# Optimization experiments

Measured on AMD Instinct MI355X. Metric: run time of the kernel, lower is better.

Reference implementation:

```python
import jax, jax.numpy as jnp
import numpy as np

DEPTH = 24
DLAT = 80      # latent_dim
H = 8          # latent_heads
DH = 64        # latent_dim_head
INNER = H * DH # 512
FFD = 2 * DLAT # FeedForward mult=2 -> 160
B = 64         # hardcoded in forward reshape
N = 128        # hardcoded max_num_nodes
MHD = 20       # multi_hop_max_dist
EF = 3         # edge feature count (meaned over by edge encoder)
EPS = 1e-5


def _ln(x, g, b):
    m = x.mean(-1, keepdims=True)
    v = ((x - m) ** 2).mean(-1, keepdims=True)
    return (x - m) / jnp.sqrt(v + EPS) * g + b


def setup_inputs() -> dict:
    key = jax.random.key(0)
    ks = jax.random.split(key, 24)
    std = 0.02 / np.sqrt(DEPTH)
    inp = {}
    # integer graph inputs
    inp['spatial_pos'] = jax.random.randint(ks[0], (B, N, N), 0, 40, dtype=jnp.int32)
    inp['edge_input'] = jax.random.randint(ks[1], (B, N, N, MHD, EF), 0, 64, dtype=jnp.int32)
    inp['x_nodes'] = jax.random.randint(ks[2], (B, N), 0, 64, dtype=jnp.int32)
    inp['indeg'] = jax.random.randint(ks[3], (B, N), 0, 64, dtype=jnp.int32)
    inp['outdeg'] = jax.random.randint(ks[4], (B, N), 0, 64, dtype=jnp.int32)
    # embedding tables (init_params: Embedding std=0.02)
    inp['atom_emb'] = 0.02 * jax.random.normal(ks[5], (64, DLAT), dtype=jnp.float32)
    inp['indeg_emb'] = 0.02 * jax.random.normal(ks[6], (64, DLAT), dtype=jnp.float32)
    inp['outdeg_emb'] = 0.02 * jax.random.normal(ks[7], (64, DLAT), dtype=jnp.float32)
    inp['edge_emb'] = 0.02 * jax.random.normal(ks[8], (64, 1), dtype=jnp.float32)
    inp['edge_dis_w'] = 0.02 * jax.random.normal(ks[9], (40,), dtype=jnp.float32)
    inp['spatial_emb'] = 0.02 * jax.random.normal(ks[10], (40, 1), dtype=jnp.float32)
    # per-layer stacked params (init_params: Linear std=0.02/sqrt(depth), bias 0)
    inp['ln1_g'] = jnp.ones((DEPTH, DLAT), jnp.float32)
    inp['ln1_b'] = jnp.zeros((DEPTH, DLAT), jnp.float32)
    inp['Wq'] = std * jax.random.normal(ks[11], (DEPTH, DLAT, INNER), dtype=jnp.float32)
    inp['Wkv'] = std * jax.random.normal(ks[12], (DEPTH, DLAT, 2 * INNER), dtype=jnp.float32)
    inp['Wo'] = std * jax.random.normal(ks[13], (DEPTH, INNER, DLAT), dtype=jnp.float32)
    inp['bo'] = jnp.zeros((DEPTH, DLAT), jnp.float32)
    inp['ln2_g'] = jnp.ones((DEPTH, DLAT), jnp.float32)
    inp['ln2_b'] = jnp.zeros((DEPTH, DLAT), jnp.float32)
    inp['W1'] = std * jax.random.normal(ks[14], (DEPTH, DLAT, FFD), dtype=jnp.float32)
    inp['b1'] = jnp.zeros((DEPTH, FFD), jnp.float32)
    inp['W2'] = std * jax.random.normal(ks[15], (DEPTH, FFD, DLAT), dtype=jnp.float32)
    inp['b2'] = jnp.zeros((DEPTH, DLAT), jnp.float32)
    # final head: LayerNorm + Linear(latent_dim, 1)
    inp['lnf_g'] = jnp.ones((DLAT,), jnp.float32)
    inp['lnf_b'] = jnp.zeros((DLAT,), jnp.float32)
    inp['Wf'] = std * jax.random.normal(ks[16], (DLAT, 1), dtype=jnp.float32)
    inp['bf'] = jnp.zeros((1,), jnp.float32)
    return inp


def reference(spatial_pos, edge_input, x_nodes, indeg, outdeg,
              atom_emb, indeg_emb, outdeg_emb, edge_emb, edge_dis_w, spatial_emb,
              ln1_g, ln1_b, Wq, Wkv, Wo, bo, ln2_g, ln2_b, W1, b1, W2, b2,
              lnf_g, lnf_b, Wf, bf):
    # --- graph structural bias ---
    sp_bias = spatial_emb[spatial_pos, 0]                       # [B,N,N]
    sp = jnp.where(spatial_pos == 0, 1, spatial_pos)
    sp = jnp.where(sp > 1, sp - 1, sp)
    sp = jnp.clip(sp, 0, MHD)
    e = edge_emb[edge_input, 0].mean(axis=-1)                   # [B,N,N,MHD] (mean over edge feats)
    e = (e * edge_dis_w[:MHD]).sum(-1) / sp.astype(jnp.float32) # per-hop scale, sum hops, normalize
    bias = e + sp_bias                                          # [B,N,N]
    # --- node embeddings ---
    x = atom_emb[x_nodes] + indeg_emb[indeg] + outdeg_emb[outdeg]  # [B,N,DLAT]
    scale = DH ** -0.5

    def layer(x, p):
        g1, be1, wq, wkv, wo, bo_, g2, be2, w1, bb1, w2, bb2 = p
        h = _ln(x, g1, be1)
        q = (h @ wq).reshape(B, N, H, DH)
        kv = h @ wkv
        k = kv[..., :INNER].reshape(B, N, H, DH)
        v = kv[..., INNER:].reshape(B, N, H, DH)
        sim = jnp.einsum('bihd,bjhd->bhij', q, k) * scale + bias[:, None]
        a = jax.nn.softmax(sim, axis=-1)
        o = jnp.einsum('bhij,bjhd->bihd', a, v).reshape(B, N, INNER)
        x = o @ wo + bo_ + x
        h = _ln(x, g2, be2)
        x = jax.nn.gelu(h @ w1 + bb1, approximate=False) @ w2 + bb2 + x
        return x, None

    x, _ = jax.lax.scan(layer, x, (ln1_g, ln1_b, Wq, Wkv, Wo, bo, ln2_g, ln2_b, W1, b1, W2, b2))
    pooled = x.mean(axis=1)                                     # Reduce 'b n d -> b d'
    return _ln(pooled, lnf_g, lnf_b) @ Wf + bf                  # [B,1]
```

## Files before the change

### kernel.cpp

```cpp
#include <hip/hip_runtime.h>
#include <math.h>

#define BDIM 64
#define NNODE 128
#define DLAT 80
#define NHEAD 8
#define DH 64
#define INNER 512
#define FFD 160
#define DEPTH 24
#define MROWS (BDIM * NNODE)

using bf16x8 = __attribute__((ext_vector_type(8))) short;
using f32x4  = __attribute__((ext_vector_type(4))) float;

#define MFMA(a, b, c) __builtin_amdgcn_mfma_f32_16x16x32_bf16((a), (b), (c), 0, 0, 0)

static __device__ __forceinline__ short f2bf(float f) {
    union { float f; unsigned u; } v; v.f = f;
    unsigned r = v.u + 0x7fffu + ((v.u >> 16) & 1u);
    return (short)(r >> 16);
}

__global__ __launch_bounds__(256) void wconv_kernel(
    const float* __restrict__ in, short* __restrict__ out, int K, int N, int Kp)
{
    __shared__ float t[64][65];
    int L = blockIdx.z;
    const float* src = in + (size_t)L * K * N;
    short* dst = out + (size_t)L * N * Kp;
    int n0 = blockIdx.x * 64, k0 = blockIdx.y * 64;
    int tx = threadIdx.x & 63, ty = threadIdx.x >> 6;
    for (int ki = ty; ki < 64; ki += 4) {
        int k = k0 + ki, n = n0 + tx;
        t[ki][tx] = (k < K && n < N) ? src[(size_t)k * N + n] : 0.f;
    }
    __syncthreads();
    for (int ni = ty; ni < 64; ni += 4) {
        int n = n0 + ni, k = k0 + tx;
        if (n < N && k < Kp) dst[(size_t)n * Kp + k] = f2bf(t[tx][ni]);
    }
}

__global__ __launch_bounds__(256) void bias_kernel(
    const int* __restrict__ spp, const int* __restrict__ ei,
    const float* __restrict__ edge_emb, const float* __restrict__ edw,
    const float* __restrict__ sp_emb, float* __restrict__ biasb)
{
    __shared__ float ee[64], ew[20], se[40];
    int tid = threadIdx.x;
    if (tid < 64) ee[tid] = edge_emb[tid];
    if (tid < 20) ew[tid] = edw[tid];
    if (tid < 40) se[tid] = sp_emb[tid];
    __syncthreads();

    int idx = blockIdx.x * 256 + tid;
    int spv = spp[idx];
    float spb = se[spv];
    int sp = min(20, max(1, spv - 1));

    const int4* p = (const int4*)(ei + (size_t)idx * 60);
    int e[60];
#pragma unroll
    for (int t = 0; t < 15; ++t) {
        int4 v = p[t];
        e[4*t+0] = v.x; e[4*t+1] = v.y; e[4*t+2] = v.z; e[4*t+3] = v.w;
    }
    float acc = 0.f;
#pragma unroll
    for (int m = 0; m < 20; ++m) {
        float s = ee[e[3*m]] + ee[e[3*m+1]] + ee[e[3*m+2]];
        acc += s * ew[m];
    }
    biasb[idx] = acc * (1.0f/3.0f) / (float)sp + spb;
}

__global__ __launch_bounds__(256) void node_emb_kernel(
    const int* __restrict__ xn, const int* __restrict__ ind, const int* __restrict__ outd,
    const float* __restrict__ ae, const float* __restrict__ ie, const float* __restrict__ oe,
    float* __restrict__ x)
{
    int idx = blockIdx.x * 256 + threadIdx.x;
    int e = idx / DLAT, d = idx % DLAT;
    x[idx] = ae[xn[e]*DLAT + d] + ie[ind[e]*DLAT + d] + oe[outd[e]*DLAT + d];
}

__global__ __launch_bounds__(256, 2) void attnfull_kernel(
    const float* __restrict__ xin, const float* __restrict__ biasb,
    const short* __restrict__ Wq_t, const short* __restrict__ Wkv_t,
    const float* __restrict__ g1, const float* __restrict__ be1,
    short* __restrict__ obuf)
{
    extern __shared__ short smem[];
    short* lnx = smem;
    short* qh  = smem + 13312;
    short* kh  = smem + 22528;
    short* vth = smem + 31744;
    short* ph  = smem;

    int tid = threadIdx.x;
    int lane = tid & 63, w = tid >> 6, l15 = lane & 15, lk = lane >> 4;
    int b = blockIdx.x >> 3, h = blockIdx.x & 7;
    const float* xb = xin + (size_t)b * NNODE * DLAT;

    {
        int row = tid >> 1, sub = tid & 1;
        const float* xr = xb + row * DLAT + sub * 40;
        float4 v[10];
#pragma unroll
        for (int i = 0; i < 10; ++i) v[i] = *(const float4*)(xr + i * 4);
        float s = 0.f;
#pragma unroll
        for (int i = 0; i < 10; ++i) s += v[i].x + v[i].y + v[i].z + v[i].w;
        s += __shfl_xor(s, 1);
        float mean = s * 0.0125f;
        float var = 0.f;
#pragma unroll
        for (int i = 0; i < 10; ++i) {
            float d;
            d = v[i].x - mean; var += d * d;
            d = v[i].y - mean; var += d * d;
            d = v[i].z - mean; var += d * d;
            d = v[i].w - mean; var += d * d;
        }
        var += __shfl_xor(var, 1);
        float rstd = 1.0f / sqrtf(var * 0.0125f + 1e-5f);
        short* dst = lnx + row * 104 + sub * 40;
#pragma unroll
        for (int i = 0; i < 10; ++i) {
            int c = sub * 40 + i * 4;
            float4 g4 = *(const float4*)(g1 + c);
            float4 b4 = *(const float4*)(be1 + c);
            short4 o;
            o.x = f2bf((v[i].x - mean) * rstd * g4.x + b4.x);
            o.y = f2bf((v[i].y - mean) * rstd * g4.y + b4.y);
            o.z = f2bf((v[i].z - mean) * rstd * g4.z + b4.z);
            o.w = f2bf((v[i].w - mean) * rstd * g4.w + b4.w);
            *(short4*)(dst + i * 4) = o;
        }
        short4 z4; z4.x = z4.y = z4.z = z4.w = 0;
        *(short4*)(lnx + row * 104 + 80 + sub * 8) = z4;
        *(short4*)(lnx + row * 104 + 84 + sub * 8) = z4;
    }
    __syncthreads();

    {
        bf16x8 a[2][3];
#pragma unroll
        for (int i = 0; i < 2; ++i)
#pragma unroll
            for (int ss = 0; ss < 3; ++ss)
                a[i][ss] = *(const bf16x8*)(lnx + ((w * 2 + i) * 16 + l15) * 104 + lk * 8 + ss * 32);

        {
            f32x4 acc[2][4] = {};
#pragma unroll
            for (int ss = 0; ss < 3; ++ss)
#pragma unroll
                for (int nf = 0; nf < 4; ++nf) {
                    bf16x8 bv = *(const bf16x8*)(Wq_t + (size_t)(h * 64 + nf * 16 + l15) * 96 + lk * 8 + ss * 32);
                    acc[0][nf] = MFMA(a[0][ss], bv, acc[0][nf]);
                    acc[1][nf] = MFMA(a[1][ss], bv, acc[1][nf]);
                }
#pragma unroll
            for (int i = 0; i < 2; ++i)
#pragma unroll
                for (int nf = 0; nf < 4; ++nf)
#pragma unroll
                    for (int r = 0; r < 4; ++r)
                        qh[((w * 2 + i) * 16 + lk * 4 + r) * 72 + nf * 16 + l15] = f2bf(acc[i][nf][r]);
        }
        {
            f32x4 acc[2][4] = {};
#pragma unroll
            for (int ss = 0; ss < 3; ++ss)
#pragma unroll
                for (int nf = 0; nf < 4; ++nf) {
                    bf16x8 bv = *(const bf16x8*)(Wkv_t + (size_t)(h * 64 + nf * 16 + l15) * 96 + lk * 8 + ss * 32);
                    acc[0][nf] = MFMA(a[0][ss], bv, acc[0][nf]);
                    acc[1][nf] = MFMA(a[1][ss], bv, acc[1][nf]);
                }
#pragma unroll
            for (int i = 0; i < 2; ++i)
#pragma unroll
                for (int nf = 0; nf < 4; ++nf)
#pragma unroll
                    for (int r = 0; r < 4; ++r)
                        kh[((w * 2 + i) * 16 + lk * 4 + r) * 72 + nf * 16 + l15] = f2bf(acc[i][nf][r]);
        }
        {
            f32x4 acc[2][4] = {};
#pragma unroll
            for (int ss = 0; ss < 3; ++ss)
#pragma unroll
                for (int nf = 0; nf < 4; ++nf) {
                    bf16x8 bv = *(const bf16x8*)(Wkv_t + (size_t)(INNER + h * 64 + nf * 16 + l15) * 96 + lk * 8 + ss * 32);
                    acc[0][nf] = MFMA(a[0][ss], bv, acc[0][nf]);
                    acc[1][nf] = MFMA(a[1][ss], bv, acc[1][nf]);
                }
#pragma unroll
            for (int i = 0; i < 2; ++i)
#pragma unroll
                for (int nf = 0; nf < 4; ++nf)
#pragma unroll
                    for (int r = 0; r < 4; ++r)
                        vth[(nf * 16 + l15) * 136 + (w * 2 + i) * 16 + lk * 4 + r] = f2bf(acc[i][nf][r]);
        }
    }
    __syncthreads();

    float breg[2][8][4];
    {
        const float* bp = biasb + ((size_t)b * NNODE + w * 32) * NNODE;
#pragma unroll
        for (int i = 0; i < 2; ++i)
#pragma unroll
            for (int jf = 0; jf < 8; ++jf)
#pragma unroll
                for (int r = 0; r < 4; ++r)
                    breg[i][jf][r] = bp[(i * 16 + lk * 4 + r) * NNODE + jf * 16 + l15];
    }

    f32x4 sc[2][8] = {};
#pragma unroll
    for (int ss = 0; ss < 2; ++ss) {
        bf16x8 qa0 = *(const bf16x8*)(qh + ((w * 2) * 16 + l15) * 72 + lk * 8 + ss * 32);
        bf16x8 qa1 = *(const bf16x8*)(qh + ((w * 2 + 1) * 16 + l15) * 72 + lk * 8 + ss * 32);
#pragma unroll
        for (int jf = 0; jf < 8; ++jf) {
            bf16x8 bv = *(const bf16x8*)(kh + (jf * 16 + l15) * 72 + lk * 8 + ss * 32);
            sc[0][jf] = MFMA(qa0, bv, sc[0][jf]);
            sc[1][jf] = MFMA(qa1, bv, sc[1][jf]);
        }
    }
    __syncthreads();

    float rinv[2][4];
#pragma unroll
    for (int i = 0; i < 2; ++i)
#pragma unroll
    for (int r = 0; r < 4; ++r) {
        float sv[8];
#pragma unroll
        for (int jf = 0; jf < 8; ++jf) sv[jf] = sc[i][jf][r] * 0.125f + breg[i][jf][r];
        float mx = sv[0];
#pragma unroll
        for (int jf = 1; jf < 8; ++jf) mx = fmaxf(mx, sv[jf]);
        mx = fmaxf(mx, __shfl_xor(mx, 1));
        mx = fmaxf(mx, __shfl_xor(mx, 2));
        mx = fmaxf(mx, __shfl_xor(mx, 4));
        mx = fmaxf(mx, __shfl_xor(mx, 8));
        float e[8], sum = 0.f;
#pragma unroll
        for (int jf = 0; jf < 8; ++jf) { e[jf] = __expf(sv[jf] - mx); sum += e[jf]; }
        sum += __shfl_xor(sum, 1);
        sum += __shfl_xor(sum, 2);
        sum += __shfl_xor(sum, 4);
        sum += __shfl_xor(sum, 8);
        rinv[i][r] = 1.0f / sum;
        int row = (w * 2 + i) * 16 + lk * 4 + r;
#pragma unroll
        for (int jf = 0; jf < 8; ++jf)
            ph[row * 136 + jf * 16 + l15] = f2bf(e[jf]);
    }
    __syncthreads();

    f32x4 o[2][4] = {};
#pragma unroll
    for (int ks = 0; ks < 4; ++ks) {
        bf16x8 pa0 = *(const bf16x8*)(ph + ((w * 2) * 16 + l15) * 136 + lk * 8 + ks * 32);
        bf16x8 pa1 = *(const bf16x8*)(ph + ((w * 2 + 1) * 16 + l15) * 136 + lk * 8 + ks * 32);
#pragma unroll
        for (int nf = 0; nf < 4; ++nf) {
            bf16x8 bv = *(const bf16x8*)(vth + (nf * 16 + l15) * 136 + lk * 8 + ks * 32);
            o[0][nf] = MFMA(pa0, bv, o[0][nf]);
            o[1][nf] = MFMA(pa1, bv, o[1][nf]);
        }
    }
#pragma unroll
    for (int i = 0; i < 2; ++i)
#pragma unroll
    for (int nf = 0; nf < 4; ++nf)
#pragma unroll
    for (int r = 0; r < 4; ++r) {
        int row = (w * 2 + i) * 16 + lk * 4 + r;
        obuf[((size_t)b * NNODE + row) * INNER + h * 64 + nf * 16 + l15] =
            f2bf(o[i][nf][r] * rinv[i][r]);
    }
}

__global__ __launch_bounds__(512, 2) void tail_kernel(
    const short* __restrict__ obuf, const float* __restrict__ xin,
    const short* __restrict__ Wo_t, const float* __restrict__ boL,
    const float* __restrict__ g2, const float* __restrict__ be2,
    const short* __restrict__ W1_t, const float* __restrict__ b1L,
    const short* __restrict__ W2_t, const float* __restrict__ b2L,
    float* __restrict__ xout)
{
    __shared__ short obs[32 * 520];
    __shared__ float xmid[32 * 84];
    __shared__ short h2s[32 * 104];
    __shared__ short ffhs[32 * 168];

    int tid = threadIdx.x;
    int lane = tid & 63, w = tid >> 6, l15 = lane & 15, lk = lane >> 4;
    int b = blockIdx.x >> 2, qq = blockIdx.x & 3;
    int R0 = qq * 32;
    int wr = w >> 2, wn = w & 3;

    {
        int row = tid >> 4, cs = (tid & 15) * 32;
        const short* src = obuf + ((size_t)b * NNODE + R0 + row) * INNER + cs;
        short* dst = obs + row * 520 + cs;
#pragma unroll
        for (int q = 0; q < 4; ++q)
            *(uint4*)(dst + q * 8) = *(const uint4*)(src + q * 8);
    }
    __syncthreads();

    const int st5[4] = {0, 2, 3, 4}, cn5[4] = {2, 1, 1, 1};
    const int st10[4] = {0, 3, 6, 8}, cn10[4] = {3, 3, 2, 2};

    {
        int n0 = st5[wn], nc = cn5[wn];
        f32x4 acc[2] = {};
#pragma unroll 4
        for (int ks = 0; ks < 16; ++ks) {
            bf16x8 aa = *(const bf16x8*)(obs + (wr * 16 + l15) * 520 + lk * 8 + ks * 32);
#pragma unroll
            for (int j = 0; j < 2; ++j)
                if (j < nc) {
                    bf16x8 bv = *(const bf16x8*)(Wo_t + (size_t)((n0 + j) * 16 + l15) * INNER + lk * 8 + ks * 32);
                    acc[j] = MFMA(aa, bv, acc[j]);
                }
        }
#pragma unroll
        for (int j = 0; j < 2; ++j)
            if (j < nc)
#pragma unroll
                for (int r = 0; r < 4; ++r) {
                    int row = wr * 16 + lk * 4 + r, col = (n0 + j) * 16 + l15;
                    xmid[row * 84 + col] = acc[j][r] + boL[col] +
                        xin[((size_t)b * NNODE + R0 + row) * DLAT + col];
                }
    }
    __syncthreads();

    {
        int row = tid >> 4, sub = tid & 15;
        float v[5];
#pragma unroll
        for (int e = 0; e < 5; ++e) v[e] = xmid[row * 84 + sub * 5 + e];
        float s = v[0] + v[1] + v[2] + v[3] + v[4];
        s += __shfl_xor(s, 1); s += __shfl_xor(s, 2);
        s += __shfl_xor(s, 4); s += __shfl_xor(s, 8);
        float mean = s * 0.0125f;
        float var = 0.f;
#pragma unroll
        for (int e = 0; e < 5; ++e) { float d = v[e] - mean; var += d * d; }
        var += __shfl_xor(var, 1); var += __shfl_xor(var, 2);
        var += __shfl_xor(var, 4); var += __shfl_xor(var, 8);
        float rstd = 1.0f / sqrtf(var * 0.0125f + 1e-5f);
#pragma unroll
        for (int e = 0; e < 5; ++e) {
            int c = sub * 5 + e;
            h2s[row * 104 + c] = f2bf((v[e] - mean) * rstd * g2[c] + be2[c]);
        }
        if (sub < 4) {
            short4 z4; z4.x = z4.y = z4.z = z4.w = 0;
            *(short4*)(h2s + row * 104 + 80 + sub * 4) = z4;
        }
    }
    __syncthreads();

    {
        int n0 = st10[wn], nc = cn10[wn];
        f32x4 acc[3] = {};
#pragma unroll
        for (int ss = 0; ss < 3; ++ss) {
            bf16x8 aa = *(const bf16x8*)(h2s + (wr * 16 + l15) * 104 + lk * 8 + ss * 32);
#pragma unroll
            for (int j = 0; j < 3; ++j)
                if (j < nc) {
                    bf16x8 bv = *(const bf16x8*)(W1_t + (size_t)((n0 + j) * 16 + l15) * 96 + lk * 8 + ss * 32);
                    acc[j] = MFMA(aa, bv, acc[j]);
                }
        }
#pragma unroll
        for (int j = 0; j < 3; ++j)
            if (j < nc)
#pragma unroll
                for (int r = 0; r < 4; ++r) {
                    int row = wr * 16 + lk * 4 + r, c = (n0 + j) * 16 + l15;
                    float vv = acc[j][r] + b1L[c];
                    vv = 0.5f * vv * (1.0f + erff(vv * 0.70710678118654752f));
                    ffhs[row * 168 + c] = f2bf(vv);
                }
    }
    __syncthreads();

    {
        int n0 = st5[wn], nc = cn5[wn];
        f32x4 acc[2] = {};
#pragma unroll
        for (int ks = 0; ks < 5; ++ks) {
            bf16x8 aa = *(const bf16x8*)(ffhs + (wr * 16 + l15) * 168 + lk * 8 + ks * 32);
#pragma unroll
            for (int j = 0; j < 2; ++j)
                if (j < nc) {
                    bf16x8 bv = *(const bf16x8*)(W2_t + (size_t)((n0 + j) * 16 + l15) * FFD + lk * 8 + ks * 32);
                    acc[j] = MFMA(aa, bv, acc[j]);
                }
        }
#pragma unroll
        for (int j = 0; j < 2; ++j)
            if (j < nc)
#pragma unroll
                for (int r = 0; r < 4; ++r) {
                    int row = wr * 16 + lk * 4 + r, col = (n0 + j) * 16 + l15;
                    xout[((size_t)b * NNODE + R0 + row) * DLAT + col] =
                        acc[j][r] + b2L[col] + xmid[row * 84 + col];
                }
    }
}

__global__ __launch_bounds__(128) void final_kernel(
    const float* __restrict__ x, const float* __restrict__ g, const float* __restrict__ bta,
    const float* __restrict__ Wf, const float* __restrict__ bf, float* __restrict__ out)
{
    int bb = blockIdx.x;
    int t = threadIdx.x;
    __shared__ float pd[DLAT];
    __shared__ float red[2];
    __shared__ float rbuf[128];

    if (t < DLAT) {
        float s = 0.f;
        for (int n = 0; n < NNODE; ++n) s += x[((size_t)bb * NNODE + n) * DLAT + t];
        pd[t] = s * (1.0f / NNODE);
    }
    __syncthreads();
    if (t == 0) {
        float m = 0.f;
        for (int k = 0; k < DLAT; ++k) m += pd[k];
        m /= DLAT;
        float v = 0.f;
        for (int k = 0; k < DLAT; ++k) { float d = pd[k] - m; v += d * d; }
        v /= DLAT;
        red[0] = m; red[1] = 1.0f / sqrtf(v + 1e-5f);
    }
    __syncthreads();
    float contrib = 0.f;
    if (t < DLAT)
        contrib = ((pd[t] - red[0]) * red[1] * g[t] + bta[t]) * Wf[t];
    rbuf[t] = contrib;
    __syncthreads();
    if (t == 0) {
        float s = 0.f;
        for (int k = 0; k < DLAT; ++k) s += rbuf[k];
        out[bb] = s + bf[0];
    }
}

extern "C" void kernel_launch(void* const* d_in, const int* in_sizes, int n_in,
                              void* d_out, int out_size, void* d_ws, size_t ws_size,
                              hipStream_t stream)
{
    const int*   spatial_pos = (const int*)  d_in[0];
    const int*   edge_input  = (const int*)  d_in[1];
    const int*   x_nodes     = (const int*)  d_in[2];
    const int*   indeg       = (const int*)  d_in[3];
    const int*   outdeg      = (const int*)  d_in[4];
    const float* atom_emb    = (const float*)d_in[5];
    const float* indeg_emb   = (const float*)d_in[6];
    const float* outdeg_emb  = (const float*)d_in[7];
    const float* edge_emb    = (const float*)d_in[8];
    const float* edge_dis_w  = (const float*)d_in[9];
    const float* spatial_emb = (const float*)d_in[10];
    const float* ln1_g = (const float*)d_in[11];
    const float* ln1_b = (const float*)d_in[12];
    const float* Wq    = (const float*)d_in[13];
    const float* Wkv   = (const float*)d_in[14];
    const float* Wo    = (const float*)d_in[15];
    const float* bo    = (const float*)d_in[16];
    const float* ln2_g = (const float*)d_in[17];
    const float* ln2_b = (const float*)d_in[18];
    const float* W1    = (const float*)d_in[19];
    const float* b1    = (const float*)d_in[20];
    const float* W2    = (const float*)d_in[21];
    const float* b2    = (const float*)d_in[22];
    const float* lnf_g = (const float*)d_in[23];
    const float* lnf_b = (const float*)d_in[24];
    const float* Wf    = (const float*)d_in[25];
    const float* bf    = (const float*)d_in[26];

    char* wsb = (char*)d_ws;
    float* biasb = (float*)(wsb + 0);
    float* x0    = (float*)(wsb + 4194304);
    float* x1    = (float*)(wsb + 6815744);
    short* obuf  = (short*)(wsb + 9437184);
    short* Wq_t  = (short*)(wsb + 17825792);
    short* Wkv_t = (short*)(wsb + 20185088);
    short* Wo_t  = (short*)(wsb + 24903680);
    short* W1_t  = (short*)(wsb + 26869760);
    short* W2_t  = (short*)(wsb + 27607040);

    static const int ATTN_LDS = 80896;
    hipFuncSetAttribute((const void*)attnfull_kernel,
                        hipFuncAttributeMaxDynamicSharedMemorySize, ATTN_LDS);

    wconv_kernel<<<dim3(8, 2, 24), 256, 0, stream>>>(Wq,  Wq_t,  80, 512, 96);
    wconv_kernel<<<dim3(16, 2, 24), 256, 0, stream>>>(Wkv, Wkv_t, 80, 1024, 96);
    wconv_kernel<<<dim3(2, 8, 24), 256, 0, stream>>>(Wo,  Wo_t,  512, 80, 512);
    wconv_kernel<<<dim3(3, 2, 24), 256, 0, stream>>>(W1,  W1_t,  80, 160, 96);
    wconv_kernel<<<dim3(2, 3, 24), 256, 0, stream>>>(W2,  W2_t,  160, 80, 160);

    bias_kernel<<<4096, 256, 0, stream>>>(spatial_pos, edge_input, edge_emb,
                                          edge_dis_w, spatial_emb, biasb);
    node_emb_kernel<<<2560, 256, 0, stream>>>(x_nodes, indeg, outdeg,
                                              atom_emb, indeg_emb, outdeg_emb, x0);

    for (int L = 0; L < DEPTH; ++L) {
        const float* xin  = (L & 1) ? x1 : x0;
        float*       xout = (L & 1) ? x0 : x1;
        attnfull_kernel<<<512, 256, ATTN_LDS, stream>>>(
            xin, biasb,
            Wq_t + (size_t)L * 512 * 96, Wkv_t + (size_t)L * 1024 * 96,
            ln1_g + L * DLAT, ln1_b + L * DLAT, obuf);
        tail_kernel<<<256, 512, 0, stream>>>(
            obuf, xin,
            Wo_t + (size_t)L * 80 * 512, bo + L * DLAT,
            ln2_g + L * DLAT, ln2_b + L * DLAT,
            W1_t + (size_t)L * 160 * 96, b1 + L * FFD,
            W2_t + (size_t)L * 80 * 160, b2 + L * DLAT,
            xout);
    }

    final_kernel<<<BDIM, 128, 0, stream>>>(x0, lnf_g, lnf_b, Wf, bf, (float*)d_out);
}
```

Measured before the change: 1.521 ms.

## Move LN1 into previous layer's tail kernel and widen attention to 512 threads

LayerNorm-1 now runs at the end of the previous layer's tail kernel, or in a new ln1_kernel before the first layer, and writes bf16 normalized activations to a global buffer. The attention kernel no longer normalizes every row once per head and can use less LDS. The attention kernel now runs 8 waves of 16 rows each, with lower per-thread register use and a staged, coalesced output store through LDS. The tail kernel reads obuf directly from global memory instead of staging it in LDS. This trades an extra global lnx buffer and more global A-operand loads in the Wo GEMM for higher occupancy and less redundant LN work.

New measurement: 1.529 ms. Within noise of the previous version (+0.5%).

```diff
diff --git a/kernel.cpp b/kernel.cpp
--- a/kernel.cpp
+++ b/kernel.cpp
@@ -85,164 +85,148 @@
     x[idx] = ae[xn[e]*DLAT + d] + ie[ind[e]*DLAT + d] + oe[outd[e]*DLAT + d];
 }
 
-__global__ __launch_bounds__(256, 2) void attnfull_kernel(
-    const float* __restrict__ xin, const float* __restrict__ biasb,
+__global__ __launch_bounds__(256) void ln1_kernel(
+    const float* __restrict__ x, const float* __restrict__ g,
+    const float* __restrict__ be, short* __restrict__ lnx)
+{
+    int row = blockIdx.x * 128 + (threadIdx.x >> 1), sub = threadIdx.x & 1;
+    const float* xr = x + (size_t)row * DLAT + sub * 40;
+    float4 v[10];
+#pragma unroll
+    for (int i = 0; i < 10; ++i) v[i] = *(const float4*)(xr + i * 4);
+    float s = 0.f;
+#pragma unroll
+    for (int i = 0; i < 10; ++i) s += v[i].x + v[i].y + v[i].z + v[i].w;
+    s += __shfl_xor(s, 1);
+    float mean = s * 0.0125f;
+    float var = 0.f;
+#pragma unroll
+    for (int i = 0; i < 10; ++i) {
+        float d;
+        d = v[i].x - mean; var += d * d;
+        d = v[i].y - mean; var += d * d;
+        d = v[i].z - mean; var += d * d;
+        d = v[i].w - mean; var += d * d;
+    }
+    var += __shfl_xor(var, 1);
+    float rstd = 1.0f / sqrtf(var * 0.0125f + 1e-5f);
+    short* dst = lnx + (size_t)row * 96 + sub * 40;
+#pragma unroll
+    for (int i = 0; i < 10; ++i) {
+        int c = sub * 40 + i * 4;
+        float4 g4 = *(const float4*)(g + c);
+        float4 b4 = *(const float4*)(be + c);
+        short4 o;
+        o.x = f2bf((v[i].x - mean) * rstd * g4.x + b4.x);
+        o.y = f2bf((v[i].y - mean) * rstd * g4.y + b4.y);
+        o.z = f2bf((v[i].z - mean) * rstd * g4.z + b4.z);
+        o.w = f2bf((v[i].w - mean) * rstd * g4.w + b4.w);
+        *(short4*)(dst + i * 4) = o;
+    }
+    short4 z4; z4.x = z4.y = z4.z = z4.w = 0;
+    *(short4*)(lnx + (size_t)row * 96 + 80 + sub * 8) = z4;
+    *(short4*)(lnx + (size_t)row * 96 + 84 + sub * 8) = z4;
+}
+
+__global__ __launch_bounds__(512, 4) void attn2_kernel(
+    const short* __restrict__ lnx, const float* __restrict__ biasb,
     const short* __restrict__ Wq_t, const short* __restrict__ Wkv_t,
-    const float* __restrict__ g1, const float* __restrict__ be1,
     short* __restrict__ obuf)
 {
     extern __shared__ short smem[];
-    short* lnx = smem;
-    short* qh  = smem + 13312;
-    short* kh  = smem + 22528;
-    short* vth = smem + 31744;
+    short* qh  = smem;
+    short* kh  = smem + 9216;
+    short* vth = smem + 18432;
     short* ph  = smem;
+    short* ot  = smem + 18432;
 
     int tid = threadIdx.x;
     int lane = tid & 63, w = tid >> 6, l15 = lane & 15, lk = lane >> 4;
     int b = blockIdx.x >> 3, h = blockIdx.x & 7;
-    const float* xb = xin + (size_t)b * NNODE * DLAT;
-
-    {
-        int row = tid >> 1, sub = tid & 1;
-        const float* xr = xb + row * DLAT + sub * 40;
-        float4 v[10];
-#pragma unroll
-        for (int i = 0; i < 10; ++i) v[i] = *(const float4*)(xr + i * 4);
-        float s = 0.f;
-#pragma unroll
-        for (int i = 0; i < 10; ++i) s += v[i].x + v[i].y + v[i].z + v[i].w;
-        s += __shfl_xor(s, 1);
-        float mean = s * 0.0125f;
-        float var = 0.f;
-#pragma unroll
-        for (int i = 0; i < 10; ++i) {
-            float d;
-            d = v[i].x - mean; var += d * d;
-            d = v[i].y - mean; var += d * d;
-            d = v[i].z - mean; var += d * d;
-            d = v[i].w - mean; var += d * d;
-        }
-        var += __shfl_xor(var, 1);
-        float rstd = 1.0f / sqrtf(var * 0.0125f + 1e-5f);
-        short* dst = lnx + row * 104 + sub * 40;
-#pragma unroll
-        for (int i = 0; i < 10; ++i) {
-            int c = sub * 40 + i * 4;
-            float4 g4 = *(const float4*)(g1 + c);
-            float4 b4 = *(const float4*)(be1 + c);
-            short4 o;
-            o.x = f2bf((v[i].x - mean) * rstd * g4.x + b4.x);
-            o.y = f2bf((v[i].y - mean) * rstd * g4.y + b4.y);
-            o.z = f2bf((v[i].z - mean) * rstd * g4.z + b4.z);
-            o.w = f2bf((v[i].w - mean) * rstd * g4.w + b4.w);
-            *(short4*)(dst + i * 4) = o;
-        }
-        short4 z4; z4.x = z4.y = z4.z = z4.w = 0;
-        *(short4*)(lnx + row * 104 + 80 + sub * 8) = z4;
-        *(short4*)(lnx + row * 104 + 84 + sub * 8) = z4;
-    }
-    __syncthreads();
-
-    {
-        bf16x8 a[2][3];
-#pragma unroll
-        for (int i = 0; i < 2; ++i)
+
+    float breg[8][4];
+    {
+        const float* bp = biasb + ((size_t)b * NNODE + w * 16) * NNODE;
+#pragma unroll
+        for (int jf = 0; jf < 8; ++jf)
+#pragma unroll
+            for (int r = 0; r < 4; ++r)
+                breg[jf][r] = bp[(lk * 4 + r) * NNODE + jf * 16 + l15];
+    }
+
+    {
+        const short* lb = lnx + (size_t)b * NNODE * 96;
+        bf16x8 a[3];
+#pragma unroll
+        for (int ss = 0; ss < 3; ++ss)
+            a[ss] = *(const bf16x8*)(lb + (w * 16 + l15) * 96 + ss * 32 + lk * 8);
+
+        {
+            f32x4 acc[4] = {};
 #pragma unroll
             for (int ss = 0; ss < 3; ++ss)
-                a[i][ss] = *(const bf16x8*)(lnx + ((w * 2 + i) * 16 + l15) * 104 + lk * 8 + ss * 32);
-
+#pragma unroll
+                for (int nf = 0; nf < 4; ++nf) {
+                    bf16x8 bv = *(const bf16x8*)(Wq_t + (size_t)(h * 64 + nf * 16 + l15) * 96 + ss * 32 + lk * 8);
+                    acc[nf] = MFMA(a[ss], bv, acc[nf]);
+                }
+#pragma unroll
+            for (int nf = 0; nf < 4; ++nf)
+#pragma unroll
+                for (int r = 0; r < 4; ++r)
+                    qh[(w * 16 + lk * 4 + r) * 72 + nf * 16 + l15] = f2bf(acc[nf][r]);
+        }
         {
-            f32x4 acc[2][4] = {};
+            f32x4 acc[4] = {};
 #pragma unroll
             for (int ss = 0; ss < 3; ++ss)
 #pragma unroll
                 for (int nf = 0; nf < 4; ++nf) {
-                    bf16x8 bv = *(const bf16x8*)(Wq_t + (size_t)(h * 64 + nf * 16 + l15) * 96 + lk * 8 + ss * 32);
-                    acc[0][nf] = MFMA(a[0][ss], bv, acc[0][nf]);
-                    acc[1][nf] = MFMA(a[1][ss], bv, acc[1][nf]);
-                }
-#pragma unroll
-            for (int i = 0; i < 2; ++i)
-#pragma unroll
-                for (int nf = 0; nf < 4; ++nf)
-#pragma unroll
-                    for (int r = 0; r < 4; ++r)
-                        qh[((w * 2 + i) * 16 + lk * 4 + r) * 72 + nf * 16 + l15] = f2bf(acc[i][nf][r]);
+                    bf16x8 bv = *(const bf16x8*)(Wkv_t + (size_t)(h * 64 + nf * 16 + l15) * 96 + ss * 32 + lk * 8);
+                    acc[nf] = MFMA(a[ss], bv, acc[nf]);
+                }
+#pragma unroll
+            for (int nf = 0; nf < 4; ++nf)
+#pragma unroll
+                for (int r = 0; r < 4; ++r)
+                    kh[(w * 16 + lk * 4 + r) * 72 + nf * 16 + l15] = f2bf(acc[nf][r]);
         }
         {
-            f32x4 acc[2][4] = {};
+            f32x4 acc[4] = {};
 #pragma unroll
             for (int ss = 0; ss < 3; ++ss)
 #pragma unroll
                 for (int nf = 0; nf < 4; ++nf) {
-                    bf16x8 bv = *(const bf16x8*)(Wkv_t + (size_t)(h * 64 + nf * 16 + l15) * 96 + lk * 8 + ss * 32);
-                    acc[0][nf] = MFMA(a[0][ss], bv, acc[0][nf]);
-                    acc[1][nf] = MFMA(a[1][ss], bv, acc[1][nf]);
-                }
-#pragma unroll
-            for (int i = 0; i < 2; ++i)
-#pragma unroll
-                for (int nf = 0; nf < 4; ++nf)
-#pragma unroll
-                    for (int r = 0; r < 4; ++r)
-                        kh[((w * 2 + i) * 16 + lk * 4 + r) * 72 + nf * 16 + l15] = f2bf(acc[i][nf][r]);
-        }
-        {
-            f32x4 acc[2][4] = {};
-#pragma unroll
-            for (int ss = 0; ss < 3; ++ss)
-#pragma unroll
-                for (int nf = 0; nf < 4; ++nf) {
-                    bf16x8 bv = *(const bf16x8*)(Wkv_t + (size_t)(INNER + h * 64 + nf * 16 + l15) * 96 + lk * 8 + ss * 32);
-                    acc[0][nf] = MFMA(a[0][ss], bv, acc[0][nf]);
-                    acc[1][nf] = MFMA(a[1][ss], bv, acc[1][nf]);
-                }
-#pragma unroll
-            for (int i = 0; i < 2; ++i)
-#pragma unroll
-                for (int nf = 0; nf < 4; ++nf)
-#pragma unroll
-                    for (int r = 0; r < 4; ++r)
-                        vth[(nf * 16 + l15) * 136 + (w * 2 + i) * 16 + lk * 4 + r] = f2bf(acc[i][nf][r]);
-        }
-    }
-    __syncthreads();
-
-    float breg[2][8][4];
-    {
-        const float* bp = biasb + ((size_t)b * NNODE + w * 32) * NNODE;
-#pragma unroll
-        for (int i = 0; i < 2; ++i)
-#pragma unroll
-            for (int jf = 0; jf < 8; ++jf)
+                    bf16x8 bv = *(const bf16x8*)(Wkv_t + (size_t)(INNER + h * 64 + nf * 16 + l15) * 96 + ss * 32 + lk * 8);
+                    acc[nf] = MFMA(a[ss], bv, acc[nf]);
+                }
+#pragma unroll
+            for (int nf = 0; nf < 4; ++nf)
 #pragma unroll
                 for (int r = 0; r < 4; ++r)
-                    breg[i][jf][r] = bp[(i * 16 + lk * 4 + r) * NNODE + jf * 16 + l15];
-    }
-
-    f32x4 sc[2][8] = {};
+                    vth[(nf * 16 + l15) * 136 + w * 16 + lk * 4 + r] = f2bf(acc[nf][r]);
+        }
+    }
+    __syncthreads();
+
+    f32x4 sc[8] = {};
 #pragma unroll
     for (int ss = 0; ss < 2; ++ss) {
-        bf16x8 qa0 = *(const bf16x8*)(qh + ((w * 2) * 16 + l15) * 72 + lk * 8 + ss * 32);
-        bf16x8 qa1 = *(const bf16x8*)(qh + ((w * 2 + 1) * 16 + l15) * 72 + lk * 8 + ss * 32);
+        bf16x8 qa = *(const bf16x8*)(qh + (w * 16 + l15) * 72 + ss * 32 + lk * 8);
 #pragma unroll
         for (int jf = 0; jf < 8; ++jf) {
-            bf16x8 bv = *(const bf16x8*)(kh + (jf * 16 + l15) * 72 + lk * 8 + ss * 32);
-            sc[0][jf] = MFMA(qa0, bv, sc[0][jf]);
-            sc[1][jf] = MFMA(qa1, bv, sc[1][jf]);
-        }
-    }
-    __syncthreads();
-
-    float rinv[2][4];
-#pragma unroll
-    for (int i = 0; i < 2; ++i)
+            bf16x8 bv = *(const bf16x8*)(kh + (jf * 16 + l15) * 72 + ss * 32 + lk * 8);
+            sc[jf] = MFMA(qa, bv, sc[jf]);
+        }
+    }
+    __syncthreads();
+
+    float rinv[4];
 #pragma unroll
     for (int r = 0; r < 4; ++r) {
         float sv[8];
 #pragma unroll
-        for (int jf = 0; jf < 8; ++jf) sv[jf] = sc[i][jf][r] * 0.125f + breg[i][jf][r];
+        for (int jf = 0; jf < 8; ++jf) sv[jf] = sc[jf][r] * 0.125f + breg[jf][r];
         float mx = sv[0];
 #pragma unroll
         for (int jf = 1; jf < 8; ++jf) mx = fmaxf(mx, sv[jf]);
@@ -257,47 +241,53 @@
         sum += __shfl_xor(sum, 2);
         sum += __shfl_xor(sum, 4);
         sum += __shfl_xor(sum, 8);
-        rinv[i][r] = 1.0f / sum;
-        int row = (w * 2 + i) * 16 + lk * 4 + r;
+        rinv[r] = 1.0f / sum;
+        int row = w * 16 + lk * 4 + r;
 #pragma unroll
         for (int jf = 0; jf < 8; ++jf)
             ph[row * 136 + jf * 16 + l15] = f2bf(e[jf]);
     }
     __syncthreads();
 
-    f32x4 o[2][4] = {};
+    f32x4 o[4] = {};
 #pragma unroll
     for (int ks = 0; ks < 4; ++ks) {
-        bf16x8 pa0 = *(const bf16x8*)(ph + ((w * 2) * 16 + l15) * 136 + lk * 8 + ks * 32);
-        bf16x8 pa1 = *(const bf16x8*)(ph + ((w * 2 + 1) * 16 + l15) * 136 + lk * 8 + ks * 32);
+        bf16x8 pa = *(const bf16x8*)(ph + (w * 16 + l15) * 136 + ks * 32 + lk * 8);
 #pragma unroll
         for (int nf = 0; nf < 4; ++nf) {
-            bf16x8 bv = *(const bf16x8*)(vth + (nf * 16 + l15) * 136 + lk * 8 + ks * 32);
-            o[0][nf] = MFMA(pa0, bv, o[0][nf]);
-            o[1][nf] = MFMA(pa1, bv, o[1][nf]);
-        }
-    }
-#pragma unroll
-    for (int i = 0; i < 2; ++i)
+            bf16x8 bv = *(const bf16x8*)(vth + (nf * 16 + l15) * 136 + ks * 32 + lk * 8);
+            o[nf] = MFMA(pa, bv, o[nf]);
+        }
+    }
+    __syncthreads();
+
 #pragma unroll
     for (int nf = 0; nf < 4; ++nf)
 #pragma unroll
-    for (int r = 0; r < 4; ++r) {
-        int row = (w * 2 + i) * 16 + lk * 4 + r;
-        obuf[((size_t)b * NNODE + row) * INNER + h * 64 + nf * 16 + l15] =
-            f2bf(o[i][nf][r] * rinv[i][r]);
-    }
-}
-
-__global__ __launch_bounds__(512, 2) void tail_kernel(
+        for (int r = 0; r < 4; ++r)
+            ot[(w * 16 + lk * 4 + r) * 68 + nf * 16 + l15] = f2bf(o[nf][r] * rinv[r]);
+    __syncthreads();
+
+    {
+        int row = tid >> 2, q4 = tid & 3;
+        const short* src = ot + row * 68 + q4 * 16;
+        short* dst = obuf + ((size_t)b * NNODE + row) * INNER + h * 64 + q4 * 16;
+#pragma unroll
+        for (int qq = 0; qq < 4; ++qq)
+            *(uint2*)(dst + qq * 4) = *(const uint2*)(src + qq * 4);
+    }
+}
+
+__global__ __launch_bounds__(512, 2) void tail2_kernel(
     const short* __restrict__ obuf, const float* __restrict__ xin,
     const short* __restrict__ Wo_t, const float* __restrict__ boL,
     const float* __restrict__ g2, const float* __restrict__ be2,
     const short* __restrict__ W1_t, const float* __restrict__ b1L,
     const short* __restrict__ W2_t, const float* __restrict__ b2L,
-    float* __restrict__ xout)
-{
-    __shared__ short obs[32 * 520];
+    float* __restrict__ xout,
+    const float* __restrict__ g1n, const float* __restrict__ be1n,
+    short* __restrict__ lnx)
+{
     __shared__ float xmid[32 * 84];
     __shared__ short h2s[32 * 104];
     __shared__ short ffhs[32 * 168];
@@ -308,38 +298,30 @@
     int R0 = qq * 32;
     int wr = w >> 2, wn = w & 3;
 
-    {
-        int row = tid >> 4, cs = (tid & 15) * 32;
-        const short* src = obuf + ((size_t)b * NNODE + R0 + row) * INNER + cs;
-        short* dst = obs + row * 520 + cs;
-#pragma unroll
-        for (int q = 0; q < 4; ++q)
-            *(uint4*)(dst + q * 8) = *(const uint4*)(src + q * 8);
-    }
-    __syncthreads();
-
-    const int st5[4] = {0, 2, 3, 4}, cn5[4] = {2, 1, 1, 1};
-    const int st10[4] = {0, 3, 6, 8}, cn10[4] = {3, 3, 2, 2};
-
-    {
-        int n0 = st5[wn], nc = cn5[wn];
+    int n0_5 = (wn == 0) ? 0 : (wn + 1);
+    int nc_5 = (wn == 0) ? 2 : 1;
+    int n0_10 = (wn < 2) ? wn * 3 : 6 + (wn - 2) * 2;
+    int nc_10 = (wn < 2) ? 3 : 2;
+
+    {
+        const short* og = obuf + ((size_t)b * NNODE + R0) * INNER;
         f32x4 acc[2] = {};
 #pragma unroll 4
         for (int ks = 0; ks < 16; ++ks) {
-            bf16x8 aa = *(const bf16x8*)(obs + (wr * 16 + l15) * 520 + lk * 8 + ks * 32);
+            bf16x8 aa = *(const bf16x8*)(og + (wr * 16 + l15) * INNER + lk * 8 + ks * 32);
 #pragma unroll
             for (int j = 0; j < 2; ++j)
-                if (j < nc) {
-                    bf16x8 bv = *(const bf16x8*)(Wo_t + (size_t)((n0 + j) * 16 + l15) * INNER + lk * 8 + ks * 32);
+                if (j < nc_5) {
+                    bf16x8 bv = *(const bf16x8*)(Wo_t + (size_t)((n0_5 + j) * 16 + l15) * INNER + lk * 8 + ks * 32);
                     acc[j] = MFMA(aa, bv, acc[j]);
                 }
         }
 #pragma unroll
         for (int j = 0; j < 2; ++j)
-            if (j < nc)
+            if (j < nc_5)
 #pragma unroll
                 for (int r = 0; r < 4; ++r) {
-                    int row = wr * 16 + lk * 4 + r, col = (n0 + j) * 16 + l15;
+                    int row = wr * 16 + lk * 4 + r, col = (n0_5 + j) * 16 + l15;
                     xmid[row * 84 + col] = acc[j][r] + boL[col] +
                         xin[((size_t)b * NNODE + R0 + row) * DLAT + col];
                 }
@@ -374,24 +356,23 @@
     __syncthreads();
 
     {
-        int n0 = st10[wn], nc = cn10[wn];
         f32x4 acc[3] = {};
 #pragma unroll
         for (int ss = 0; ss < 3; ++ss) {
             bf16x8 aa = *(const bf16x8*)(h2s + (wr * 16 + l15) * 104 + lk * 8 + ss * 32);
 #pragma unroll
             for (int j = 0; j < 3; ++j)
-                if (j < nc) {
-                    bf16x8 bv = *(const bf16x8*)(W1_t + (size_t)((n0 + j) * 16 + l15) * 96 + lk * 8 + ss * 32);
+                if (j < nc_10) {
+                    bf16x8 bv = *(const bf16x8*)(W1_t + (size_t)((n0_10 + j) * 16 + l15) * 96 + lk * 8 + ss * 32);
                     acc[j] = MFMA(aa, bv, acc[j]);
                 }
         }
 #pragma unroll
         for (int j = 0; j < 3; ++j)
-            if (j < nc)
+            if (j < nc_10)
 #pragma unroll
                 for (int r = 0; r < 4; ++r) {
-                    int row = wr * 16 + lk * 4 + r, c = (n0 + j) * 16 + l15;
+                    int row = wr * 16 + lk * 4 + r, c = (n0_10 + j) * 16 + l15;
                     float vv = acc[j][r] + b1L[c];
                     vv = 0.5f * vv * (1.0f + erff(vv * 0.70710678118654752f));
                     ffhs[row * 168 + c] = f2bf(vv);
@@ -400,27 +381,52 @@
     __syncthreads();
 
     {
-        int n0 = st5[wn], nc = cn5[wn];
         f32x4 acc[2] = {};
 #pragma unroll
         for (int ks = 0; ks < 5; ++ks) {
             bf16x8 aa = *(const bf16x8*)(ffhs + (wr * 16 + l15) * 168 + lk * 8 + ks * 32);
 #pragma unroll
             for (int j = 0; j < 2; ++j)
-                if (j < nc) {
-                    bf16x8 bv = *(const bf16x8*)(W2_t + (size_t)((n0 + j) * 16 + l15) * FFD + lk * 8 + ks * 32);
+                if (j < nc_5) {
+                    bf16x8 bv = *(const bf16x8*)(W2_t + (size_t)((n0_5 + j) * 16 + l15) * FFD + lk * 8 + ks * 32);
                     acc[j] = MFMA(aa, bv, acc[j]);
                 }
         }
 #pragma unroll
         for (int j = 0; j < 2; ++j)
-            if (j < nc)
+            if (j < nc_5)
 #pragma unroll
                 for (int r = 0; r < 4; ++r) {
-                    int row = wr * 16 + lk * 4 + r, col = (n0 + j) * 16 + l15;
-                    xout[((size_t)b * NNODE + R0 + row) * DLAT + col] =
-                        acc[j][r] + b2L[col] + xmid[row * 84 + col];
-                }
+                    int row = wr * 16 + lk * 4 + r, col = (n0_5 + j) * 16 + l15;
+                    float vv = acc[j][r] + b2L[col] + xmid[row * 84 + col];
+                    xout[((size_t)b * NNODE + R0 + row) * DLAT + col] = vv;
+                    xmid[row * 84 + col] = vv;
+                }
+    }
+    __syncthreads();
+
+    if (g1n) {
+        int row = tid >> 4, sub = tid & 15;
+        float v[5];
+#pragma unroll
+        for (int e = 0; e < 5; ++e) v[e] = xmid[row * 84 + sub * 5 + e];
+        float s = v[0] + v[1] + v[2] + v[3] + v[4];
+        s += __shfl_xor(s, 1); s += __shfl_xor(s, 2);
+        s += __shfl_xor(s, 4); s += __shfl_xor(s, 8);
+        float mean = s * 0.0125f;
+        float var = 0.f;
+#pragma unroll
+        for (int e = 0; e < 5; ++e) { float d = v[e] - mean; var += d * d; }
+        var += __shfl_xor(var, 1); var += __shfl_xor(var, 2);
+        var += __shfl_xor(var, 4); var += __shfl_xor(var, 8);
+        float rstd = 1.0f / sqrtf(var * 0.0125f + 1e-5f);
+        short* lr = lnx + ((size_t)b * NNODE + R0 + row) * 96;
+#pragma unroll
+        for (int e = 0; e < 5; ++e) {
+            int c = sub * 5 + e;
+            lr[c] = f2bf((v[e] - mean) * rstd * g1n[c] + be1n[c]);
+        }
+        if (sub < 8) { lr[80 + sub * 2] = 0; lr[81 + sub * 2] = 0; }
     }
 }
 
@@ -504,9 +510,10 @@
     short* Wo_t  = (short*)(wsb + 24903680);
     short* W1_t  = (short*)(wsb + 26869760);
     short* W2_t  = (short*)(wsb + 27607040);
-
-    static const int ATTN_LDS = 80896;
-    hipFuncSetAttribute((const void*)attnfull_kernel,
+    short* lnx   = (short*)(wsb + 28221440);
+
+    static const int ATTN_LDS = 54272;
+    hipFuncSetAttribute((const void*)attn2_kernel,
                         hipFuncAttributeMaxDynamicSharedMemorySize, ATTN_LDS);
 
     wconv_kernel<<<dim3(8, 2, 24), 256, 0, stream>>>(Wq,  Wq_t,  80, 512, 96);
@@ -519,21 +526,24 @@
                                           edge_dis_w, spatial_emb, biasb);
     node_emb_kernel<<<2560, 256, 0, stream>>>(x_nodes, indeg, outdeg,
                                               atom_emb, indeg_emb, outdeg_emb, x0);
+    ln1_kernel<<<64, 256, 0, stream>>>(x0, ln1_g, ln1_b, lnx);
 
     for (int L = 0; L < DEPTH; ++L) {
         const float* xin  = (L & 1) ? x1 : x0;
         float*       xout = (L & 1) ? x0 : x1;
-        attnfull_kernel<<<512, 256, ATTN_LDS, stream>>>(
-            xin, biasb,
+        attn2_kernel<<<512, 512, ATTN_LDS, stream>>>(
+            lnx, biasb,
             Wq_t + (size_t)L * 512 * 96, Wkv_t + (size_t)L * 1024 * 96,
-            ln1_g + L * DLAT, ln1_b + L * DLAT, obuf);
-        tail_kernel<<<256, 512, 0, stream>>>(
+            obuf);
+        const float* g1n  = (L < DEPTH - 1) ? (ln1_g + (L + 1) * DLAT) : nullptr;
+        const float* be1n = (L < DEPTH - 1) ? (ln1_b + (L + 1) * DLAT) : nullptr;
+        tail2_kernel<<<256, 512, 0, stream>>>(
             obuf, xin,
             Wo_t + (size_t)L * 80 * 512, bo + L * DLAT,
             ln2_g + L * DLAT, ln2_b + L * DLAT,
             W1_t + (size_t)L * 160 * 96, b1 + L * FFD,
             W2_t + (size_t)L * 80 * 160, b2 + L * DLAT,
-            xout);
+            xout, g1n, be1n, lnx);
     }
 
     final_kernel<<<BDIM, 128, 0, stream>>>(x0, lnf_g, lnf_b, Wf, bf, (float*)d_out);
```
